# Performance work log

Hardware: AMD Instinct MI355X
Metric: run time of the kernel (lower is better)

## Reference

```python
import jax, jax.numpy as jnp
import numpy as np

BS, SEQ, DIM = 4, 4096, 4096
N_HEADS, N_KV_HEADS = 32, 8
HEAD_DIM = DIM // N_HEADS  # 128
ROPE_THETA = 10000.0


def _rope_tables(seq_len, head_dim, dtype=jnp.float32):
    # LLaMA-style interleaved-pair rotary tables: [seq, head_dim//2]
    inv_freq = 1.0 / (ROPE_THETA ** (np.arange(0, head_dim, 2, dtype=np.float32) / head_dim))
    t = np.arange(seq_len, dtype=np.float32)
    freqs = np.outer(t, inv_freq)  # [seq, head_dim//2]
    return jnp.asarray(np.cos(freqs), dtype), jnp.asarray(np.sin(freqs), dtype)


def setup_inputs() -> dict:
    key = jax.random.key(0)
    kx, kq, kk, kv = jax.random.split(key, 4)
    scale = 0.02
    x = jax.random.normal(kx, (BS, SEQ, DIM), dtype=jnp.float32)
    wq = jax.random.normal(kq, (N_HEADS * HEAD_DIM, DIM), dtype=jnp.float32) * scale
    wk = jax.random.normal(kk, (N_KV_HEADS * HEAD_DIM, DIM), dtype=jnp.float32) * scale
    wv = jax.random.normal(kv, (N_KV_HEADS * HEAD_DIM, DIM), dtype=jnp.float32) * scale
    cos, sin = _rope_tables(SEQ, HEAD_DIM)
    return {"x": x, "wq": wq, "wk": wk, "wv": wv, "cos": cos, "sin": sin}


def _apply_rotary(t, cos, sin):
    # t: [b, s, h, d]; cos/sin: [s, d//2]; interleaved (even, odd) pairs
    t1 = t[..., 0::2]
    t2 = t[..., 1::2]
    c = cos[None, :, None, :]
    s = sin[None, :, None, :]
    r1 = t1 * c - t2 * s
    r2 = t1 * s + t2 * c
    out = jnp.stack([r1, r2], axis=-1)  # [b,s,h,d//2,2]
    return out.reshape(t.shape)


def reference(x, wq, wk, wv, cos, sin):
    bs, seq_len, _ = x.shape
    # torch nn.Linear: y = x @ W.T, W is [out, in]
    q = jnp.einsum('bsi,oi->bso', x, wq).reshape(bs, seq_len, N_HEADS, HEAD_DIM)
    k = jnp.einsum('bsi,oi->bso', x, wk).reshape(bs, seq_len, N_KV_HEADS, HEAD_DIM)
    v = jnp.einsum('bsi,oi->bso', x, wv).reshape(bs, seq_len, N_KV_HEADS, HEAD_DIM)
    q = _apply_rotary(q, cos, sin)
    k = _apply_rotary(k, cos, sin)
    # transpose(1, 2).contiguous() -> [bs, heads, seq, head_dim]
    return (jnp.transpose(q, (0, 2, 1, 3)),
            jnp.transpose(k, (0, 2, 1, 3)),
            jnp.transpose(v, (0, 2, 1, 3)))
```

## Files before the change

kernel.cpp:

```cpp
#include <hip/hip_runtime.h>
#include <stdint.h>

#define SEQ 4096
#define DIM 4096
#define NH 32
#define NKV 8
#define HD 128

typedef __bf16 bf16x8 __attribute__((ext_vector_type(8)));
typedef __bf16 bf16x4 __attribute__((ext_vector_type(4)));
typedef float f32x4 __attribute__((ext_vector_type(4)));

__global__ __launch_bounds__(512, 2)
void qkv_rope_kernel(const float* __restrict__ x,
                     const float* __restrict__ wq,
                     const float* __restrict__ wk,
                     const float* __restrict__ wv,
                     const float* __restrict__ cosT,
                     const float* __restrict__ sinT,
                     float* __restrict__ out) {
    __shared__ __align__(16) char smem[2 * 32768];

    const int t = threadIdx.x;
    const int lane = t & 63;
    const int w = t >> 6;
    const int bn = blockIdx.x;
    const int bm = blockIdx.y;

    const float* W;
    int n_mat;
    if (bn < 16)      { W = wq; n_mat = bn << 8; }
    else if (bn < 20) { W = wk; n_mat = (bn - 16) << 8; }
    else              { W = wv; n_mat = (bn - 20) << 8; }

    const int m0 = bm << 8;

    const int srow = t >> 3;
    const int sc   = t & 7;
    const int sdso = srow * 64 + (((sc >> 1) ^ (srow & 3)) * 16) + (sc & 1) * 8;

    const float* ga = x + (size_t)(m0 + srow) * DIM + sc * 4;
    const float* gb = W + (size_t)(n_mat + srow) * DIM + sc * 4;

    const int wm = (w & 1) << 7;
    const int wn = (w >> 1) << 6;
    const int fr = lane & 15;
    const int q4 = lane >> 4;
    const int sw = (q4 ^ (fr & 3)) * 16;

    int offA[8], offB[4];
#pragma unroll
    for (int i = 0; i < 8; i++) offA[i] = (wm + i * 16 + fr) * 64 + sw;
#pragma unroll
    for (int j = 0; j < 4; j++) offB[j] = 16384 + (wn + j * 16 + fr) * 64 + sw;

    f32x4 acc[8][4];
#pragma unroll
    for (int i = 0; i < 8; i++)
#pragma unroll
        for (int j = 0; j < 4; j++)
            acc[i][j] = (f32x4){0.f, 0.f, 0.f, 0.f};

    f32x4 rA[4], rB[4];

#define STAGE_LOAD() do {                                                   \
    _Pragma("unroll")                                                       \
    for (int p = 0; p < 4; p++) {                                           \
        rA[p] = *(const f32x4*)(ga + (size_t)p * 64 * DIM);                 \
        rB[p] = *(const f32x4*)(gb + (size_t)p * 64 * DIM);                 \
    }                                                                       \
    ga += 32; gb += 32;                                                     \
} while (0)

#define STAGE_WRITE(buf) do {                                               \
    char* dst = smem + (buf) * 32768;                                       \
    _Pragma("unroll")                                                       \
    for (int p = 0; p < 4; p++) {                                           \
        bf16x4 va, vb;                                                      \
        _Pragma("unroll")                                                   \
        for (int e = 0; e < 4; e++) {                                       \
            va[e] = (__bf16)rA[p][e];                                       \
            vb[e] = (__bf16)rB[p][e];                                       \
        }                                                                   \
        *(bf16x4*)(dst + p * 4096 + sdso) = va;                             \
        *(bf16x4*)(dst + 16384 + p * 4096 + sdso) = vb;                     \
    }                                                                       \
} while (0)

#define COMPUTE(buf) do {                                                   \
    const char* srcb = smem + (buf) * 32768;                                \
    bf16x8 bfr[4];                                                          \
    _Pragma("unroll")                                                       \
    for (int j = 0; j < 4; j++) bfr[j] = *(const bf16x8*)(srcb + offB[j]);  \
    _Pragma("unroll")                                                       \
    for (int i = 0; i < 8; i++) {                                           \
        const bf16x8 af = *(const bf16x8*)(srcb + offA[i]);                 \
        _Pragma("unroll")                                                   \
        for (int j = 0; j < 4; j++)                                         \
            acc[i][j] = __builtin_amdgcn_mfma_f32_16x16x32_bf16(            \
                af, bfr[j], acc[i][j], 0, 0, 0);                            \
    }                                                                       \
} while (0)

    STAGE_LOAD();
    STAGE_WRITE(0);
    __syncthreads();

    for (int it = 0; it < 126; it += 2) {
        STAGE_LOAD();
        COMPUTE(0);
        __builtin_amdgcn_sched_barrier(0);
        STAGE_WRITE(1);
        __syncthreads();

        STAGE_LOAD();
        COMPUTE(1);
        __builtin_amdgcn_sched_barrier(0);
        STAGE_WRITE(0);
        __syncthreads();
    }
    STAGE_LOAD();
    COMPUTE(0);
    __builtin_amdgcn_sched_barrier(0);
    STAGE_WRITE(1);
    __syncthreads();
    COMPUTE(1);

    const size_t QSZ = (size_t)4 * NH * SEQ * HD;
    const size_t KSZ = (size_t)4 * NKV * SEQ * HD;
    size_t region, bstr;
    bool do_rope;
    if (bn < 16)      { region = 0;         bstr = (size_t)NH  * SEQ * HD; do_rope = true; }
    else if (bn < 20) { region = QSZ;       bstr = (size_t)NKV * SEQ * HD; do_rope = true; }
    else              { region = QSZ + KSZ; bstr = (size_t)NKV * SEQ * HD; do_rope = false; }

    const int col_l = lane & 15;
#pragma unroll
    for (int j = 0; j < 4; j++) {
        const int n_local = n_mat + wn + j * 16 + col_l;
        const int h = n_local >> 7;
        const int d = n_local & 127;
        const int fidx = d >> 1;
        const size_t base_j = region + (size_t)h * (SEQ * HD) + d;
#pragma unroll
        for (int i = 0; i < 8; i++) {
            const int mrow = m0 + wm + i * 16 + q4 * 4;
#pragma unroll
            for (int r = 0; r < 4; r++) {
                const int m = mrow + r;
                const int b = m >> 12;
                const int s = m & (SEQ - 1);
                float v = acc[i][j][r];
                if (do_rope) {
                    const float cv = cosT[s * 64 + fidx];
                    const float sv = sinT[s * 64 + fidx];
                    const float other = __shfl_xor(v, 1, 64);
                    v = (d & 1) ? fmaf(v, cv, other * sv) : fmaf(v, cv, -other * sv);
                }
                out[base_j + (size_t)b * bstr + (size_t)s * HD] = v;
            }
        }
    }
#undef STAGE_LOAD
#undef STAGE_WRITE
#undef COMPUTE
}

extern "C" void kernel_launch(void* const* d_in, const int* in_sizes, int n_in,
                              void* d_out, int out_size, void* d_ws, size_t ws_size,
                              hipStream_t stream) {
    const float* x    = (const float*)d_in[0];
    const float* wq   = (const float*)d_in[1];
    const float* wk   = (const float*)d_in[2];
    const float* wv   = (const float*)d_in[3];
    const float* cosT = (const float*)d_in[4];
    const float* sinT = (const float*)d_in[5];
    float* out = (float*)d_out;

    dim3 grid(24, 64);
    dim3 block(512);
    qkv_rope_kernel<<<grid, block, 0, stream>>>(x, wq, wk, wv, cosT, sinT, out);
}
```

Before: 2.085 ms.

## Pre-convert inputs to bf16 and pipeline GEMM with direct global-to-LDS loads

Adds a separate pass that converts x and the three weight matrices to bf16 in workspace. The main GEMM then streams bf16 tiles straight into LDS with global_load_lds, using a 64-wide K tile, a 128 KB double buffer, an XOR swizzle and a phased schedule that raises priority around the MFMA blocks. This removes the per-tile fp32 register staging and conversion from the GEMM loop and halves the operand bytes it reads. In exchange it adds a full extra read and write of the inputs, a large workspace requirement and a more fragile hand-written schedule, and it keeps the old kernel as a fallback for when the workspace is too small.

```diff
diff --git a/kernel.cpp b/kernel.cpp
--- a/kernel.cpp
+++ b/kernel.cpp
@@ -11,15 +11,46 @@
 typedef __bf16 bf16x4 __attribute__((ext_vector_type(4)));
 typedef float f32x4 __attribute__((ext_vector_type(4)));
 
+__device__ __forceinline__ void gl_lds16(const void* g, void* l) {
+    __builtin_amdgcn_global_load_lds(
+        (const __attribute__((address_space(1))) void*)g,
+        (__attribute__((address_space(3))) void*)l, 16, 0, 0);
+}
+
+__global__ __launch_bounds__(256)
+void cvt_kernel(const float* __restrict__ x,
+                const float* __restrict__ wq,
+                const float* __restrict__ wk,
+                const float* __restrict__ wv,
+                __bf16* __restrict__ xb,
+                __bf16* __restrict__ wb) {
+    const size_t NX = 16777216;
+    const size_t NQ = 4194304;
+    const size_t NK = 1048576;
+    const size_t NV = 1048576;
+    const size_t NT = NX + NQ + NK + NV;
+    for (size_t g = (size_t)blockIdx.x * 256 + threadIdx.x; g < NT;
+         g += (size_t)gridDim.x * 256) {
+        const float* s; __bf16* d; size_t off;
+        if (g < NX)                { s = x;  d = xb;            off = g; }
+        else if (g < NX + NQ)      { s = wq; d = wb;            off = g - NX; }
+        else if (g < NX + NQ + NK) { s = wk; d = wb + 16777216; off = g - NX - NQ; }
+        else                       { s = wv; d = wb + 20971520; off = g - NX - NQ - NK; }
+        const f32x4 v = *(const f32x4*)(s + off * 4);
+        bf16x4 o;
+#pragma unroll
+        for (int e = 0; e < 4; e++) o[e] = (__bf16)v[e];
+        *(bf16x4*)(d + off * 4) = o;
+    }
+}
+
 __global__ __launch_bounds__(512, 2)
-void qkv_rope_kernel(const float* __restrict__ x,
-                     const float* __restrict__ wq,
-                     const float* __restrict__ wk,
-                     const float* __restrict__ wv,
-                     const float* __restrict__ cosT,
-                     const float* __restrict__ sinT,
-                     float* __restrict__ out) {
-    __shared__ __align__(16) char smem[2 * 32768];
+void qkv8_kernel(const __bf16* __restrict__ xb,
+                 const __bf16* __restrict__ wb,
+                 const float* __restrict__ cosT,
+                 const float* __restrict__ sinT,
+                 float* __restrict__ out) {
+    extern __shared__ char sm[];
 
     const int t = threadIdx.x;
     const int lane = t & 63;
@@ -27,32 +58,38 @@
     const int bn = blockIdx.x;
     const int bm = blockIdx.y;
 
-    const float* W;
     int n_mat;
-    if (bn < 16)      { W = wq; n_mat = bn << 8; }
-    else if (bn < 20) { W = wk; n_mat = (bn - 16) << 8; }
-    else              { W = wv; n_mat = (bn - 20) << 8; }
+    if (bn < 16)      n_mat = bn << 8;
+    else if (bn < 20) n_mat = (bn - 16) << 8;
+    else              n_mat = (bn - 20) << 8;
 
     const int m0 = bm << 8;
 
-    const int srow = t >> 3;
-    const int sc   = t & 7;
-    const int sdso = srow * 64 + (((sc >> 1) ^ (srow & 3)) * 16) + (sc & 1) * 8;
-
-    const float* ga = x + (size_t)(m0 + srow) * DIM + sc * 4;
-    const float* gb = W + (size_t)(n_mat + srow) * DIM + sc * 4;
+    const int row_r = t >> 3;
+    const int colE  = ((t & 7) ^ (row_r & 7)) << 3;
+    const size_t eAbase = (size_t)(m0 + row_r) * DIM + colE;
+    const size_t eBbase = (size_t)(bn * 256 + row_r) * DIM + colE;
 
     const int wm = (w & 1) << 7;
     const int wn = (w >> 1) << 6;
     const int fr = lane & 15;
     const int q4 = lane >> 4;
-    const int sw = (q4 ^ (fr & 3)) * 16;
-
-    int offA[8], offB[4];
-#pragma unroll
-    for (int i = 0; i < 8; i++) offA[i] = (wm + i * 16 + fr) * 64 + sw;
-#pragma unroll
-    for (int j = 0; j < 4; j++) offB[j] = 16384 + (wn + j * 16 + fr) * 64 + sw;
+
+    int aoff[2][4], boff[2][2];
+#pragma unroll
+    for (int mh = 0; mh < 2; mh++)
+#pragma unroll
+        for (int i = 0; i < 4; i++) {
+            const int row = wm + mh * 64 + i * 16 + fr;
+            aoff[mh][i] = row * 128 + ((q4 * 16) ^ ((row & 7) << 4));
+        }
+#pragma unroll
+    for (int nh = 0; nh < 2; nh++)
+#pragma unroll
+        for (int j = 0; j < 2; j++) {
+            const int row = wn + nh * 32 + j * 16 + fr;
+            boff[nh][j] = 32768 + row * 128 + ((q4 * 16) ^ ((row & 7) << 4));
+        }
 
     f32x4 acc[8][4];
 #pragma unroll
@@ -61,70 +98,106 @@
         for (int j = 0; j < 4; j++)
             acc[i][j] = (f32x4){0.f, 0.f, 0.f, 0.f};
 
-    f32x4 rA[4], rB[4];
-
-#define STAGE_LOAD() do {                                                   \
-    _Pragma("unroll")                                                       \
-    for (int p = 0; p < 4; p++) {                                           \
-        rA[p] = *(const f32x4*)(ga + (size_t)p * 64 * DIM);                 \
-        rB[p] = *(const f32x4*)(gb + (size_t)p * 64 * DIM);                 \
-    }                                                                       \
-    ga += 32; gb += 32;                                                     \
-} while (0)
-
-#define STAGE_WRITE(buf) do {                                               \
-    char* dst = smem + (buf) * 32768;                                       \
-    _Pragma("unroll")                                                       \
-    for (int p = 0; p < 4; p++) {                                           \
-        bf16x4 va, vb;                                                      \
-        _Pragma("unroll")                                                   \
-        for (int e = 0; e < 4; e++) {                                       \
-            va[e] = (__bf16)rA[p][e];                                       \
-            vb[e] = (__bf16)rB[p][e];                                       \
-        }                                                                   \
-        *(bf16x4*)(dst + p * 4096 + sdso) = va;                             \
-        *(bf16x4*)(dst + 16384 + p * 4096 + sdso) = vb;                     \
-    }                                                                       \
-} while (0)
-
-#define COMPUTE(buf) do {                                                   \
-    const char* srcb = smem + (buf) * 32768;                                \
-    bf16x8 bfr[4];                                                          \
-    _Pragma("unroll")                                                       \
-    for (int j = 0; j < 4; j++) bfr[j] = *(const bf16x8*)(srcb + offB[j]);  \
-    _Pragma("unroll")                                                       \
-    for (int i = 0; i < 8; i++) {                                           \
-        const bf16x8 af = *(const bf16x8*)(srcb + offA[i]);                 \
-        _Pragma("unroll")                                                   \
-        for (int j = 0; j < 4; j++)                                         \
-            acc[i][j] = __builtin_amdgcn_mfma_f32_16x16x32_bf16(            \
-                af, bfr[j], acc[i][j], 0, 0, 0);                            \
-    }                                                                       \
-} while (0)
-
-    STAGE_LOAD();
-    STAGE_WRITE(0);
-    __syncthreads();
-
-    for (int it = 0; it < 126; it += 2) {
-        STAGE_LOAD();
-        COMPUTE(0);
-        __builtin_amdgcn_sched_barrier(0);
-        STAGE_WRITE(1);
-        __syncthreads();
-
-        STAGE_LOAD();
-        COMPUTE(1);
-        __builtin_amdgcn_sched_barrier(0);
-        STAGE_WRITE(0);
-        __syncthreads();
-    }
-    STAGE_LOAD();
-    COMPUTE(0);
-    __builtin_amdgcn_sched_barrier(0);
-    STAGE_WRITE(1);
-    __syncthreads();
-    COMPUTE(1);
+    bf16x8 Ar[8], B0r[4], B1r[4];
+
+#define LDA(MH, DB) do { _Pragma("unroll") \
+    for (int i_ = 0; i_ < 4; i_++) { \
+        Ar[i_*2]   = *(const bf16x8*)(sm + (DB)*65536 + aoff[MH][i_]); \
+        Ar[i_*2+1] = *(const bf16x8*)(sm + (DB)*65536 + (aoff[MH][i_] ^ 64)); \
+    } } while (0)
+
+#define LDB(BR, NHh, DB) do { _Pragma("unroll") \
+    for (int j_ = 0; j_ < 2; j_++) { \
+        BR[j_*2]   = *(const bf16x8*)(sm + (DB)*65536 + boff[NHh][j_]); \
+        BR[j_*2+1] = *(const bf16x8*)(sm + (DB)*65536 + (boff[NHh][j_] ^ 64)); \
+    } } while (0)
+
+#define QUAD(MH, NHh, BR) do { _Pragma("unroll") \
+    for (int i_ = 0; i_ < 4; i_++) { _Pragma("unroll") \
+        for (int j_ = 0; j_ < 2; j_++) { \
+            f32x4 c_ = acc[(MH)*4+i_][(NHh)*2+j_]; \
+            c_ = __builtin_amdgcn_mfma_f32_16x16x32_bf16(Ar[i_*2],   BR[j_*2],   c_, 0, 0, 0); \
+            c_ = __builtin_amdgcn_mfma_f32_16x16x32_bf16(Ar[i_*2+1], BR[j_*2+1], c_, 0, 0, 0); \
+            acc[(MH)*4+i_][(NHh)*2+j_] = c_; \
+        } } } while (0)
+
+#define STG_A(H, TILE, DB) do { \
+    gl_lds16(xb + eAbase + (H)*524288 + (size_t)(TILE)*64, \
+             sm + (DB)*65536 + (H)*16384 + w*1024); \
+    gl_lds16(xb + eAbase + (H)*524288 + 262144 + (size_t)(TILE)*64, \
+             sm + (DB)*65536 + (H)*16384 + 8192 + w*1024); } while (0)
+#define STG_B(H, TILE, DB) do { \
+    gl_lds16(wb + eBbase + (H)*524288 + (size_t)(TILE)*64, \
+             sm + (DB)*65536 + 32768 + (H)*16384 + w*1024); \
+    gl_lds16(wb + eBbase + (H)*524288 + 262144 + (size_t)(TILE)*64, \
+             sm + (DB)*65536 + 32768 + (H)*16384 + 8192 + w*1024); } while (0)
+
+#define PH_MID() do { \
+    asm volatile("" ::: "memory"); \
+    __builtin_amdgcn_s_barrier(); \
+    asm volatile("s_waitcnt lgkmcnt(0)" ::: "memory"); \
+    __builtin_amdgcn_sched_barrier(0); \
+    __builtin_amdgcn_s_setprio(1); } while (0)
+#define PH_END() do { \
+    __builtin_amdgcn_s_setprio(0); \
+    asm volatile("" ::: "memory"); \
+    __builtin_amdgcn_s_barrier(); \
+    asm volatile("" ::: "memory"); } while (0)
+#define PH_END_VM(N) do { \
+    __builtin_amdgcn_s_setprio(0); \
+    asm volatile("s_waitcnt vmcnt(" #N ")" ::: "memory"); \
+    __builtin_amdgcn_s_barrier(); \
+    asm volatile("" ::: "memory"); } while (0)
+
+    STG_A(0, 0, 0); STG_A(1, 0, 0); STG_B(0, 0, 0); STG_B(1, 0, 0);
+    STG_B(0, 1, 1); STG_A(0, 1, 1); STG_A(1, 1, 1);
+    asm volatile("s_waitcnt vmcnt(6)" ::: "memory");
+    __builtin_amdgcn_s_barrier();
+    asm volatile("" ::: "memory");
+
+    for (int T = 0; T < 62; T += 2) {
+        LDA(0, 0); LDB(B0r, 0, 0); STG_B(1, T + 1, 1);
+        PH_MID(); QUAD(0, 0, B0r); PH_END();
+        LDB(B1r, 1, 0);
+        PH_MID(); QUAD(0, 1, B1r); PH_END();
+        LDA(1, 0); STG_B(0, T + 2, 0); STG_B(1, T + 2, 0);
+        PH_MID(); QUAD(1, 1, B1r); PH_END();
+        STG_A(0, T + 2, 0); STG_A(1, T + 2, 0);
+        PH_MID(); QUAD(1, 0, B0r); PH_END_VM(8);
+        LDA(0, 1); LDB(B0r, 0, 1);
+        PH_MID(); QUAD(0, 0, B0r); PH_END();
+        LDB(B1r, 1, 1);
+        PH_MID(); QUAD(0, 1, B1r); PH_END();
+        LDA(1, 1); STG_B(0, T + 3, 1);
+        PH_MID(); QUAD(1, 1, B1r); PH_END();
+        STG_A(0, T + 3, 1); STG_A(1, T + 3, 1);
+        PH_MID(); QUAD(1, 0, B0r); PH_END_VM(6);
+    }
+
+    LDA(0, 0); LDB(B0r, 0, 0); STG_B(1, 63, 1);
+    PH_MID(); QUAD(0, 0, B0r); PH_END();
+    LDB(B1r, 1, 0);
+    PH_MID(); QUAD(0, 1, B1r); PH_END();
+    LDA(1, 0);
+    PH_MID(); QUAD(1, 1, B1r); PH_END();
+    PH_MID(); QUAD(1, 0, B0r); PH_END_VM(0);
+    LDA(0, 1); LDB(B0r, 0, 1);
+    PH_MID(); QUAD(0, 0, B0r); PH_END();
+    LDB(B1r, 1, 1);
+    PH_MID(); QUAD(0, 1, B1r); PH_END();
+    LDA(1, 1);
+    PH_MID(); QUAD(1, 1, B1r); PH_END();
+    PH_MID(); QUAD(1, 0, B0r);
+    __builtin_amdgcn_s_setprio(0);
+
+#undef LDA
+#undef LDB
+#undef QUAD
+#undef STG_A
+#undef STG_B
+#undef PH_MID
+#undef PH_END
+#undef PH_END_VM
 
     const size_t QSZ = (size_t)4 * NH * SEQ * HD;
     const size_t KSZ = (size_t)4 * NKV * SEQ * HD;
@@ -161,9 +234,143 @@
             }
         }
     }
-#undef STAGE_LOAD
-#undef STAGE_WRITE
-#undef COMPUTE
+}
+
+__global__ __launch_bounds__(512, 2)
+void qkv_rope_fallback(const float* __restrict__ x,
+                       const float* __restrict__ wq,
+                       const float* __restrict__ wk,
+                       const float* __restrict__ wv,
+                       const float* __restrict__ cosT,
+                       const float* __restrict__ sinT,
+                       float* __restrict__ out) {
+    __shared__ __align__(16) char smem[2 * 32768];
+
+    const int t = threadIdx.x;
+    const int lane = t & 63;
+    const int w = t >> 6;
+    const int bn = blockIdx.x;
+    const int bm = blockIdx.y;
+
+    const float* W;
+    int n_mat;
+    if (bn < 16)      { W = wq; n_mat = bn << 8; }
+    else if (bn < 20) { W = wk; n_mat = (bn - 16) << 8; }
+    else              { W = wv; n_mat = (bn - 20) << 8; }
+
+    const int m0 = bm << 8;
+    const int srow = t >> 3;
+    const int sc   = t & 7;
+    const int sdso = srow * 64 + (((sc >> 1) ^ (srow & 3)) * 16) + (sc & 1) * 8;
+
+    const float* ga = x + (size_t)(m0 + srow) * DIM + sc * 4;
+    const float* gb = W + (size_t)(n_mat + srow) * DIM + sc * 4;
+
+    const int wm = (w & 1) << 7;
+    const int wn = (w >> 1) << 6;
+    const int fr = lane & 15;
+    const int q4 = lane >> 4;
+    const int sw = (q4 ^ (fr & 3)) * 16;
+
+    int offA[8], offB[4];
+#pragma unroll
+    for (int i = 0; i < 8; i++) offA[i] = (wm + i * 16 + fr) * 64 + sw;
+#pragma unroll
+    for (int j = 0; j < 4; j++) offB[j] = 16384 + (wn + j * 16 + fr) * 64 + sw;
+
+    f32x4 acc[8][4];
+#pragma unroll
+    for (int i = 0; i < 8; i++)
+#pragma unroll
+        for (int j = 0; j < 4; j++)
+            acc[i][j] = (f32x4){0.f, 0.f, 0.f, 0.f};
+
+    f32x4 rA[4], rB[4];
+
+#define FB_LOAD() do { _Pragma("unroll") \
+    for (int p = 0; p < 4; p++) { \
+        rA[p] = *(const f32x4*)(ga + (size_t)p * 64 * DIM); \
+        rB[p] = *(const f32x4*)(gb + (size_t)p * 64 * DIM); \
+    } ga += 32; gb += 32; } while (0)
+
+#define FB_WRITE(buf) do { \
+    char* dst = smem + (buf) * 32768; \
+    _Pragma("unroll") \
+    for (int p = 0; p < 4; p++) { \
+        bf16x4 va, vb; \
+        _Pragma("unroll") \
+        for (int e = 0; e < 4; e++) { va[e] = (__bf16)rA[p][e]; vb[e] = (__bf16)rB[p][e]; } \
+        *(bf16x4*)(dst + p * 4096 + sdso) = va; \
+        *(bf16x4*)(dst + 16384 + p * 4096 + sdso) = vb; \
+    } } while (0)
+
+#define FB_COMPUTE(buf) do { \
+    const char* srcb = smem + (buf) * 32768; \
+    bf16x8 bfr[4]; \
+    _Pragma("unroll") \
+    for (int j = 0; j < 4; j++) bfr[j] = *(const bf16x8*)(srcb + offB[j]); \
+    _Pragma("unroll") \
+    for (int i = 0; i < 8; i++) { \
+        const bf16x8 af = *(const bf16x8*)(srcb + offA[i]); \
+        _Pragma("unroll") \
+        for (int j = 0; j < 4; j++) \
+            acc[i][j] = __builtin_amdgcn_mfma_f32_16x16x32_bf16(af, bfr[j], acc[i][j], 0, 0, 0); \
+    } } while (0)
+
+    FB_LOAD();
+    FB_WRITE(0);
+    __syncthreads();
+    for (int it = 0; it < 126; it += 2) {
+        FB_LOAD(); FB_COMPUTE(0);
+        __builtin_amdgcn_sched_barrier(0);
+        FB_WRITE(1); __syncthreads();
+        FB_LOAD(); FB_COMPUTE(1);
+        __builtin_amdgcn_sched_barrier(0);
+        FB_WRITE(0); __syncthreads();
+    }
+    FB_LOAD(); FB_COMPUTE(0);
+    __builtin_amdgcn_sched_barrier(0);
+    FB_WRITE(1); __syncthreads();
+    FB_COMPUTE(1);
+#undef FB_LOAD
+#undef FB_WRITE
+#undef FB_COMPUTE
+
+    const size_t QSZ = (size_t)4 * NH * SEQ * HD;
+    const size_t KSZ = (size_t)4 * NKV * SEQ * HD;
+    size_t region, bstr;
+    bool do_rope;
+    if (bn < 16)      { region = 0;         bstr = (size_t)NH  * SEQ * HD; do_rope = true; }
+    else if (bn < 20) { region = QSZ;       bstr = (size_t)NKV * SEQ * HD; do_rope = true; }
+    else              { region = QSZ + KSZ; bstr = (size_t)NKV * SEQ * HD; do_rope = false; }
+
+    const int col_l = lane & 15;
+#pragma unroll
+    for (int j = 0; j < 4; j++) {
+        const int n_local = n_mat + wn + j * 16 + col_l;
+        const int h = n_local >> 7;
+        const int d = n_local & 127;
+        const int fidx = d >> 1;
+        const size_t base_j = region + (size_t)h * (SEQ * HD) + d;
+#pragma unroll
+        for (int i = 0; i < 8; i++) {
+            const int mrow = m0 + wm + i * 16 + q4 * 4;
+#pragma unroll
+            for (int r = 0; r < 4; r++) {
+                const int m = mrow + r;
+                const int b = m >> 12;
+                const int s = m & (SEQ - 1);
+                float v = acc[i][j][r];
+                if (do_rope) {
+                    const float cv = cosT[s * 64 + fidx];
+                    const float sv = sinT[s * 64 + fidx];
+                    const float other = __shfl_xor(v, 1, 64);
+                    v = (d & 1) ? fmaf(v, cv, other * sv) : fmaf(v, cv, -other * sv);
+                }
+                out[base_j + (size_t)b * bstr + (size_t)s * HD] = v;
+            }
+        }
+    }
 }
 
 extern "C" void kernel_launch(void* const* d_in, const int* in_sizes, int n_in,
@@ -177,7 +384,21 @@
     const float* sinT = (const float*)d_in[5];
     float* out = (float*)d_out;
 
-    dim3 grid(24, 64);
-    dim3 block(512);
-    qkv_rope_kernel<<<grid, block, 0, stream>>>(x, wq, wk, wv, cosT, sinT, out);
+    const size_t XB_BYTES = (size_t)16384 * 4096 * 2;
+    const size_t WB_BYTES = (size_t)6144 * 4096 * 2;
+
+    if (ws_size >= XB_BYTES + WB_BYTES) {
+        __bf16* xb = (__bf16*)d_ws;
+        __bf16* wb = (__bf16*)((char*)d_ws + XB_BYTES);
+        static bool attr_done = false;
+        if (!attr_done) {
+            (void)hipFuncSetAttribute((const void*)qkv8_kernel,
+                                      hipFuncAttributeMaxDynamicSharedMemorySize, 131072);
+            attr_done = true;
+        }
+        cvt_kernel<<<dim3(8192), dim3(256), 0, stream>>>(x, wq, wk, wv, xb, wb);
+        qkv8_kernel<<<dim3(24, 64), dim3(512), 131072, stream>>>(xb, wb, cosT, sinT, out);
+    } else {
+        qkv_rope_fallback<<<dim3(24, 64), dim3(512), 0, stream>>>(x, wq, wk, wv, cosT, sinT, out);
+    }
 }
```

Measured after the change: 1.864 ms. -10.6%, faster.
